# Optimization experiments

Measured on AMD Instinct MI355X. Metric: run time of the kernel, lower is better.

## Reference

```python
import jax, jax.numpy as jnp
import numpy as np

MAXT = 10000
BATCH = 4096
LOG_GAMMA = float(np.log(1.02))
ALPHA = float(np.log(0.99) / 1000.0)
INIT_LOGW = float(np.log(0.248))
INIT_LOGP = float(np.log(0.001))
TEMPERATURE = 1000.0
EPS = 1e-12


def setup_inputs() -> dict:
    key = jax.random.key(0)
    k1, k2 = jax.random.split(key)
    # actions are initialized to -10 in the original module (must be << 0 so exp(a) < 1)
    acts = -10.0 * jnp.ones((MAXT,), dtype=jnp.float32)
    u1 = jax.random.uniform(k1, (MAXT, BATCH), dtype=jnp.float32)
    u2 = jax.random.uniform(k2, (MAXT, BATCH), dtype=jnp.float32)
    return {"acts": acts, "u1": u1, "u2": u2}


def _gumbel_sigmoid(logp, uu1, uu2):
    # logit = logp - log(1 - exp(logp))
    logit = logp - jnp.log1p(-jnp.exp(logp))
    noise = -jnp.log(jnp.log(uu2 + EPS) / jnp.log(uu1 + EPS) + EPS)
    soft = jax.nn.sigmoid(logit + noise)  # gumbel_temp = 1
    hard = (soft > 0.5).astype(soft.dtype)
    # straight-through: hard value, soft gradient
    return soft + jax.lax.stop_gradient(hard - soft)


def reference(acts, u1, u2):
    def step(carry, xs):
        logp, logw, alive, cumrew = carry
        a, uu1, uu2 = xs
        alive = alive * (1.0 - _gumbel_sigmoid(logp, uu1, uu2))
        f = jnp.exp(a)
        new_logw = logw + LOG_GAMMA + jnp.log(1.0 - f)
        new_logp = logp + ALPHA * f * jnp.exp(logw)
        rwd = alive * jnp.exp(new_logw / TEMPERATURE)
        return (new_logp, new_logw, alive, cumrew + rwd), None

    batch = u1.shape[1]
    init = (
        jnp.full((batch,), INIT_LOGP, dtype=jnp.float32),
        jnp.full((batch,), INIT_LOGW, dtype=jnp.float32),
        jnp.ones((batch,), dtype=jnp.float32),
        jnp.zeros((batch,), dtype=jnp.float32),
    )
    (_, _, _, cumrew), _ = jax.lax.scan(step, init, (acts, u1, u2))
    return cumrew.mean()
```

## Files before the change

### kernel.cpp

```cpp
#include <hip/hip_runtime.h>

#define MAXT 10000
#define BATCH 4096
#define NT_SETUP 512
#define SEG 20
#define TCHUNK 16
#define NYB 80
#define CUT_LOGIT -27.7f

__device__ __forceinline__ float block_exscan(float v, float* sh, int tid) {
    sh[tid] = v;
    __syncthreads();
    for (int off = 1; off < NT_SETUP; off <<= 1) {
        float x = (tid >= off) ? sh[tid - off] : 0.0f;
        __syncthreads();
        sh[tid] += x;
        __syncthreads();
    }
    float excl = (tid > 0) ? sh[tid - 1] : 0.0f;
    __syncthreads();
    return excl;
}

__global__ __launch_bounds__(NT_SETUP) void setup_kernel(
    const float* __restrict__ acts,
    float* __restrict__ gate,
    float* __restrict__ rpref,
    float* __restrict__ cbuf,
    int*   __restrict__ tcut,
    int*   __restrict__ firstfire)
{
    __shared__ float sh[NT_SETUP];
    __shared__ int   shi[NT_SETUP];
    const int tid = threadIdx.x;

    const float LOG_GAMMA = 1.9802627296e-2f;
    const float ALPHA     = -1.0050335854e-5f;
    const float INIT_LOGW = -1.3943265329f;
    const float INIT_LOGP = -6.9077552790f;

    for (int i = tid; i < BATCH; i += NT_SETUP) firstfire[i] = MAXT;

    const int t0 = tid * SEG;
    const int n  = (t0 < MAXT) ? min(SEG, MAXT - t0) : 0;

    float lsum = 0.0f;
    for (int i = 0; i < n; ++i) {
        float f = expf(acts[t0 + i]);
        lsum += LOG_GAMMA + logf(1.0f - f);
    }
    float excl = block_exscan(lsum, sh, tid);
    float run = INIT_LOGW + excl;
    for (int i = 0; i < n; ++i) {
        int t = t0 + i;
        float f = expf(acts[t]);
        float d = LOG_GAMMA + logf(1.0f - f);
        cbuf[t]  = ALPHA * f * expf(run);
        rpref[t] = expf((run + d) * (1.0f / 1000.0f));
        run += d;
    }

    float csum = 0.0f;
    for (int i = 0; i < n; ++i) csum += cbuf[t0 + i];
    excl = block_exscan(csum, sh, tid);
    float logp = INIT_LOGP + excl;
    int localFirst = MAXT;
    for (int i = 0; i < n; ++i) {
        int t = t0 + i;
        float lg = logp - log1pf(-expf(logp));
        gate[t] = expf(lg) - 1e-12f;
        if (localFirst == MAXT && lg <= CUT_LOGIT) localFirst = t;
        logp += cbuf[t];
    }
    shi[tid] = localFirst;
    __syncthreads();
    for (int off = NT_SETUP / 2; off > 0; off >>= 1) {
        if (tid < off) shi[tid] = min(shi[tid], shi[tid + off]);
        __syncthreads();
    }
    if (tid == 0) tcut[0] = shi[0];

    float rsum = 0.0f;
    for (int i = 0; i < n; ++i) rsum += rpref[t0 + i];
    excl = block_exscan(rsum, sh, tid);
    float rrun = excl;
    for (int i = 0; i < n; ++i) {
        int t = t0 + i;
        float v = rpref[t];
        rpref[t] = rrun;
        rrun += v;
    }
    if (n > 0 && (t0 + n) == MAXT) rpref[MAXT] = rrun;
}

__global__ __launch_bounds__(256) void scan_kernel(
    const float* __restrict__ u1, const float* __restrict__ u2,
    const float* __restrict__ gate, const int* __restrict__ tcutp,
    int* __restrict__ firstfire)
{
    const int tid = threadIdx.x;
    const int b4  = (blockIdx.x * 256 + tid) * 4;
    const int tcut = *tcutp;
    const float E = 1e-12f;

    int f0 = MAXT, f1 = MAXT, f2 = MAXT, f3 = MAXT;

    for (int chunk = blockIdx.y; chunk * TCHUNK < tcut; chunk += gridDim.y) {
        const int tbase = chunk * TCHUNK;
        #pragma unroll
        for (int g = 0; g < TCHUNK / 4; ++g) {
            float4 a[4], c[4];
            float gv[4];
            #pragma unroll
            for (int j = 0; j < 4; ++j) {
                const int t = tbase + g * 4 + j;
                a[j]  = *(const float4*)(u1 + (size_t)t * BATCH + b4);
                c[j]  = *(const float4*)(u2 + (size_t)t * BATCH + b4);
                gv[j] = gate[t];
            }
            #pragma unroll
            for (int j = 0; j < 4; ++j) {
                const int t = tbase + g * 4 + j;
                const float k = gv[j];
                if (__logf(c[j].x + E) > k * __logf(a[j].x + E)) f0 = min(f0, t);
                if (__logf(c[j].y + E) > k * __logf(a[j].y + E)) f1 = min(f1, t);
                if (__logf(c[j].z + E) > k * __logf(a[j].z + E)) f2 = min(f2, t);
                if (__logf(c[j].w + E) > k * __logf(a[j].w + E)) f3 = min(f3, t);
            }
        }
    }

    if (f0 != MAXT) atomicMin(firstfire + b4 + 0, f0);
    if (f1 != MAXT) atomicMin(firstfire + b4 + 1, f1);
    if (f2 != MAXT) atomicMin(firstfire + b4 + 2, f2);
    if (f3 != MAXT) atomicMin(firstfire + b4 + 3, f3);
}

__global__ __launch_bounds__(1024) void finalize_kernel(
    const int* __restrict__ firstfire, const float* __restrict__ rpref,
    float* __restrict__ out)
{
    __shared__ double ssum[1024];
    const int tid = threadIdx.x;
    double s = 0.0;
    for (int i = tid; i < BATCH; i += 1024) {
        int t = firstfire[i];
        s += (double)rpref[t];
    }
    ssum[tid] = s;
    __syncthreads();
    for (int off = 512; off > 0; off >>= 1) {
        if (tid < off) ssum[tid] += ssum[tid + off];
        __syncthreads();
    }
    if (tid == 0) out[0] = (float)(ssum[0] / (double)BATCH);
}

extern "C" void kernel_launch(void* const* d_in, const int* in_sizes, int n_in,
                              void* d_out, int out_size, void* d_ws, size_t ws_size,
                              hipStream_t stream) {
    const float* acts = (const float*)d_in[0];
    const float* u1   = (const float*)d_in[1];
    const float* u2   = (const float*)d_in[2];
    float* out = (float*)d_out;

    float* W       = (float*)d_ws;
    float* gate    = W;
    float* rpref   = W + MAXT;
    float* cbuf    = W + 2 * MAXT + 4;
    int*   tcut    = (int*)(W + 3 * MAXT + 8);
    int*   ffire   = tcut + 4;

    setup_kernel<<<1, NT_SETUP, 0, stream>>>(acts, gate, rpref, cbuf, tcut, ffire);

    dim3 grid(BATCH / (256 * 4), NYB);
    scan_kernel<<<grid, 256, 0, stream>>>(u1, u2, gate, tcut, ffire);

    finalize_kernel<<<1, 1024, 0, stream>>>(ffire, rpref, out);
}
```

Measured before the change: 315.3 us.

## Fuse setup prefix scans into scan kernel and replace atomics with per-block table

Removes the single-block setup kernel: every scan block now recomputes the logw/logp prefix scans for the actions segment by segment in shared memory and stops early once the gate odds fall below a cutoff. Per-block first-fire times go into a table indexed by blockIdx.y instead of global atomicMin, and the finalize kernel reduces over that table and recomputes the reward prefix in shared memory. This removes the serial setup launch and its global round trip, plus the atomics, at the cost of redundant per-block recomputation of the scans and a larger finalize reduction.

```diff
diff --git a/kernel.cpp b/kernel.cpp
--- a/kernel.cpp
+++ b/kernel.cpp
@@ -1,159 +1,196 @@
 #include <hip/hip_runtime.h>
+#include <limits.h>
 
 #define MAXT 10000
 #define BATCH 4096
-#define NT_SETUP 512
-#define SEG 20
+#define NYB 80
 #define TCHUNK 16
-#define NYB 80
-#define CUT_LOGIT -27.7f
-
-__device__ __forceinline__ float block_exscan(float v, float* sh, int tid) {
+#define SEGT 1536
+#define EPT 6
+#define NT2 1024
+#define SEG2 10
+#define CUT_ODDS 9.3e-13f
+
+#define LOG_GAMMA_C  1.9802627296e-2f
+#define ALPHA_C     -1.0050335854e-5f
+#define INIT_LOGW_C -1.3943265329f
+#define INIT_LOGP_C -6.9077552790f
+#define EPS_C        1e-12f
+
+__device__ __forceinline__ float block_exscan_tot(float v, float* sh, int tid,
+                                                  int n, float* tot) {
     sh[tid] = v;
     __syncthreads();
-    for (int off = 1; off < NT_SETUP; off <<= 1) {
+    for (int off = 1; off < n; off <<= 1) {
         float x = (tid >= off) ? sh[tid - off] : 0.0f;
         __syncthreads();
         sh[tid] += x;
         __syncthreads();
     }
     float excl = (tid > 0) ? sh[tid - 1] : 0.0f;
-    __syncthreads();
+    float t_ = sh[n - 1];
+    __syncthreads();
+    *tot = t_;
     return excl;
 }
 
-__global__ __launch_bounds__(NT_SETUP) void setup_kernel(
+__global__ __launch_bounds__(256) void scan_fused(
     const float* __restrict__ acts,
-    float* __restrict__ gate,
-    float* __restrict__ rpref,
-    float* __restrict__ cbuf,
-    int*   __restrict__ tcut,
-    int*   __restrict__ firstfire)
+    const float* __restrict__ u1, const float* __restrict__ u2,
+    unsigned* __restrict__ fftab)
 {
-    __shared__ float sh[NT_SETUP];
-    __shared__ int   shi[NT_SETUP];
+    __shared__ float sh[256];
+    __shared__ int   shi[256];
+    __shared__ float s_gate[SEGT];
+
     const int tid = threadIdx.x;
-
-    const float LOG_GAMMA = 1.9802627296e-2f;
-    const float ALPHA     = -1.0050335854e-5f;
-    const float INIT_LOGW = -1.3943265329f;
-    const float INIT_LOGP = -6.9077552790f;
-
-    for (int i = tid; i < BATCH; i += NT_SETUP) firstfire[i] = MAXT;
-
-    const int t0 = tid * SEG;
-    const int n  = (t0 < MAXT) ? min(SEG, MAXT - t0) : 0;
-
+    const int b4  = (blockIdx.x * 256 + tid) * 4;
+    const float E = EPS_C;
+
+    float carry_w = INIT_LOGW_C;
+    float carry_p = INIT_LOGP_C;
+    unsigned f0 = MAXT, f1 = MAXT, f2 = MAXT, f3 = MAXT;
+
+    for (int seg_base = 0; seg_base < MAXT; seg_base += SEGT) {
+        float fv[EPT], dv[EPT];
+        float lsum = 0.0f;
+        #pragma unroll
+        for (int i = 0; i < EPT; ++i) {
+            int t = seg_base + tid * EPT + i;
+            if (t < MAXT) {
+                float f = expf(acts[t]);
+                fv[i] = f;
+                dv[i] = LOG_GAMMA_C + logf(1.0f - f);
+            } else { fv[i] = 0.0f; dv[i] = 0.0f; }
+            lsum += dv[i];
+        }
+        float dtot;
+        float excl = block_exscan_tot(lsum, sh, tid, 256, &dtot);
+
+        float run = carry_w + excl;
+        float cv[EPT];
+        float csum = 0.0f;
+        #pragma unroll
+        for (int i = 0; i < EPT; ++i) {
+            cv[i] = ALPHA_C * fv[i] * expf(run);
+            run += dv[i];
+            csum += cv[i];
+        }
+        float ctot;
+        float cexcl = block_exscan_tot(csum, sh, tid, 256, &ctot);
+
+        float logp = carry_p + cexcl;
+        int localFirst = INT_MAX;
+        #pragma unroll
+        for (int i = 0; i < EPT; ++i) {
+            int t = seg_base + tid * EPT + i;
+            float el   = expf(logp);
+            float odds = el / (1.0f - el);
+            s_gate[tid * EPT + i] = odds - E;
+            if (localFirst == INT_MAX && odds <= CUT_ODDS) localFirst = t;
+            logp += cv[i];
+        }
+        shi[tid] = localFirst;
+        __syncthreads();
+        for (int off = 128; off > 0; off >>= 1) {
+            if (tid < off) shi[tid] = min(shi[tid], shi[tid + off]);
+            __syncthreads();
+        }
+        const int segcut = shi[0];
+        __syncthreads();
+
+        const int tlimit = min(segcut, MAXT);
+        for (int lc = 0; lc < SEGT / TCHUNK; ++lc) {
+            const int cg = seg_base / TCHUNK + lc;
+            if ((cg % NYB) != (int)blockIdx.y) continue;
+            const int tstart = seg_base + lc * TCHUNK;
+            if (tstart >= tlimit) break;
+            #pragma unroll
+            for (int g = 0; g < TCHUNK / 4; ++g) {
+                float4 a[4], c[4];
+                float gv[4];
+                #pragma unroll
+                for (int j = 0; j < 4; ++j) {
+                    const int t = tstart + g * 4 + j;
+                    a[j]  = *(const float4*)(u1 + (size_t)t * BATCH + b4);
+                    c[j]  = *(const float4*)(u2 + (size_t)t * BATCH + b4);
+                    gv[j] = s_gate[t - seg_base];
+                }
+                #pragma unroll
+                for (int j = 0; j < 4; ++j) {
+                    const unsigned t = (unsigned)(tstart + g * 4 + j);
+                    const float k = gv[j];
+                    if (__logf(c[j].x + E) > k * __logf(a[j].x + E)) f0 = min(f0, t);
+                    if (__logf(c[j].y + E) > k * __logf(a[j].y + E)) f1 = min(f1, t);
+                    if (__logf(c[j].z + E) > k * __logf(a[j].z + E)) f2 = min(f2, t);
+                    if (__logf(c[j].w + E) > k * __logf(a[j].w + E)) f3 = min(f3, t);
+                }
+            }
+        }
+
+        if (segcut != INT_MAX) break;
+        carry_w += dtot;
+        carry_p += ctot;
+        __syncthreads();
+    }
+
+    uint4 outv; outv.x = f0; outv.y = f1; outv.z = f2; outv.w = f3;
+    *(uint4*)(fftab + (size_t)blockIdx.y * BATCH + b4) = outv;
+}
+
+__global__ __launch_bounds__(NT2) void finalize_kernel(
+    const float* __restrict__ acts,
+    const unsigned* __restrict__ fftab,
+    float* __restrict__ out)
+{
+    __shared__ float  sh[NT2];
+    __shared__ float  rp[MAXT + 1];
+    __shared__ double sd[NT2];
+    const int tid = threadIdx.x;
+
+    const int t0 = tid * SEG2;
+    const int n  = (t0 < MAXT) ? min(SEG2, MAXT - t0) : 0;
+
+    float dv[SEG2];
     float lsum = 0.0f;
     for (int i = 0; i < n; ++i) {
         float f = expf(acts[t0 + i]);
-        lsum += LOG_GAMMA + logf(1.0f - f);
-    }
-    float excl = block_exscan(lsum, sh, tid);
-    float run = INIT_LOGW + excl;
+        dv[i] = LOG_GAMMA_C + logf(1.0f - f);
+        lsum += dv[i];
+    }
+    float dtot;
+    float excl = block_exscan_tot(lsum, sh, tid, NT2, &dtot);
+    float run = INIT_LOGW_C + excl;
+
+    float rv[SEG2];
+    float rsum = 0.0f;
     for (int i = 0; i < n; ++i) {
-        int t = t0 + i;
-        float f = expf(acts[t]);
-        float d = LOG_GAMMA + logf(1.0f - f);
-        cbuf[t]  = ALPHA * f * expf(run);
-        rpref[t] = expf((run + d) * (1.0f / 1000.0f));
-        run += d;
-    }
-
-    float csum = 0.0f;
-    for (int i = 0; i < n; ++i) csum += cbuf[t0 + i];
-    excl = block_exscan(csum, sh, tid);
-    float logp = INIT_LOGP + excl;
-    int localFirst = MAXT;
-    for (int i = 0; i < n; ++i) {
-        int t = t0 + i;
-        float lg = logp - log1pf(-expf(logp));
-        gate[t] = expf(lg) - 1e-12f;
-        if (localFirst == MAXT && lg <= CUT_LOGIT) localFirst = t;
-        logp += cbuf[t];
-    }
-    shi[tid] = localFirst;
-    __syncthreads();
-    for (int off = NT_SETUP / 2; off > 0; off >>= 1) {
-        if (tid < off) shi[tid] = min(shi[tid], shi[tid + off]);
-        __syncthreads();
-    }
-    if (tid == 0) tcut[0] = shi[0];
-
-    float rsum = 0.0f;
-    for (int i = 0; i < n; ++i) rsum += rpref[t0 + i];
-    excl = block_exscan(rsum, sh, tid);
-    float rrun = excl;
-    for (int i = 0; i < n; ++i) {
-        int t = t0 + i;
-        float v = rpref[t];
-        rpref[t] = rrun;
-        rrun += v;
-    }
-    if (n > 0 && (t0 + n) == MAXT) rpref[MAXT] = rrun;
-}
-
-__global__ __launch_bounds__(256) void scan_kernel(
-    const float* __restrict__ u1, const float* __restrict__ u2,
-    const float* __restrict__ gate, const int* __restrict__ tcutp,
-    int* __restrict__ firstfire)
-{
-    const int tid = threadIdx.x;
-    const int b4  = (blockIdx.x * 256 + tid) * 4;
-    const int tcut = *tcutp;
-    const float E = 1e-12f;
-
-    int f0 = MAXT, f1 = MAXT, f2 = MAXT, f3 = MAXT;
-
-    for (int chunk = blockIdx.y; chunk * TCHUNK < tcut; chunk += gridDim.y) {
-        const int tbase = chunk * TCHUNK;
-        #pragma unroll
-        for (int g = 0; g < TCHUNK / 4; ++g) {
-            float4 a[4], c[4];
-            float gv[4];
-            #pragma unroll
-            for (int j = 0; j < 4; ++j) {
-                const int t = tbase + g * 4 + j;
-                a[j]  = *(const float4*)(u1 + (size_t)t * BATCH + b4);
-                c[j]  = *(const float4*)(u2 + (size_t)t * BATCH + b4);
-                gv[j] = gate[t];
-            }
-            #pragma unroll
-            for (int j = 0; j < 4; ++j) {
-                const int t = tbase + g * 4 + j;
-                const float k = gv[j];
-                if (__logf(c[j].x + E) > k * __logf(a[j].x + E)) f0 = min(f0, t);
-                if (__logf(c[j].y + E) > k * __logf(a[j].y + E)) f1 = min(f1, t);
-                if (__logf(c[j].z + E) > k * __logf(a[j].z + E)) f2 = min(f2, t);
-                if (__logf(c[j].w + E) > k * __logf(a[j].w + E)) f3 = min(f3, t);
-            }
-        }
-    }
-
-    if (f0 != MAXT) atomicMin(firstfire + b4 + 0, f0);
-    if (f1 != MAXT) atomicMin(firstfire + b4 + 1, f1);
-    if (f2 != MAXT) atomicMin(firstfire + b4 + 2, f2);
-    if (f3 != MAXT) atomicMin(firstfire + b4 + 3, f3);
-}
-
-__global__ __launch_bounds__(1024) void finalize_kernel(
-    const int* __restrict__ firstfire, const float* __restrict__ rpref,
-    float* __restrict__ out)
-{
-    __shared__ double ssum[1024];
-    const int tid = threadIdx.x;
+        run += dv[i];
+        rv[i] = expf(run * 1e-3f);
+        rsum += rv[i];
+    }
+    float rtot;
+    float rexcl = block_exscan_tot(rsum, sh, tid, NT2, &rtot);
+    float rrun = rexcl;
+    for (int i = 0; i < n; ++i) { rp[t0 + i] = rrun; rrun += rv[i]; }
+    if (tid == 0) rp[MAXT] = rtot;
+    __syncthreads();
+
     double s = 0.0;
-    for (int i = tid; i < BATCH; i += 1024) {
-        int t = firstfire[i];
-        s += (double)rpref[t];
-    }
-    ssum[tid] = s;
-    __syncthreads();
-    for (int off = 512; off > 0; off >>= 1) {
-        if (tid < off) ssum[tid] += ssum[tid + off];
-        __syncthreads();
-    }
-    if (tid == 0) out[0] = (float)(ssum[0] / (double)BATCH);
+    for (int b = tid; b < BATCH; b += NT2) {
+        unsigned ff = 0xFFFFFFFFu;
+        #pragma unroll 8
+        for (int y = 0; y < NYB; ++y) ff = min(ff, fftab[(size_t)y * BATCH + b]);
+        int t = (int)min(ff, (unsigned)MAXT);
+        s += (double)rp[t];
+    }
+    sd[tid] = s;
+    __syncthreads();
+    for (int off = NT2 / 2; off > 0; off >>= 1) {
+        if (tid < off) sd[tid] += sd[tid + off];
+        __syncthreads();
+    }
+    if (tid == 0) out[0] = (float)(sd[0] / (double)BATCH);
 }
 
 extern "C" void kernel_launch(void* const* d_in, const int* in_sizes, int n_in,
@@ -164,17 +201,9 @@
     const float* u2   = (const float*)d_in[2];
     float* out = (float*)d_out;
 
-    float* W       = (float*)d_ws;
-    float* gate    = W;
-    float* rpref   = W + MAXT;
-    float* cbuf    = W + 2 * MAXT + 4;
-    int*   tcut    = (int*)(W + 3 * MAXT + 8);
-    int*   ffire   = tcut + 4;
-
-    setup_kernel<<<1, NT_SETUP, 0, stream>>>(acts, gate, rpref, cbuf, tcut, ffire);
+    unsigned* fftab = (unsigned*)d_ws;
 
     dim3 grid(BATCH / (256 * 4), NYB);
-    scan_kernel<<<grid, 256, 0, stream>>>(u1, u2, gate, tcut, ffire);
-
-    finalize_kernel<<<1, 1024, 0, stream>>>(ffire, rpref, out);
-}
+    scan_fused<<<grid, 256, 0, stream>>>(acts, u1, u2, fftab);
+    finalize_kernel<<<1, NT2, 0, stream>>>(acts, fftab, out);
+}
```

Result: faster. 291.4 us (-7.6%).
